# Performance work log

Hardware: AMD Instinct MI355X
Metric: run time of the kernel (lower is better)

## Reference

```python
import jax, jax.numpy as jnp
import numpy as np

SEQ_LENGTH = 8192
P_DIM = 128  # number of landmarks


def setup_inputs() -> dict:
    key = jax.random.key(0)
    kq, kk, kv = jax.random.split(key, 3)
    shape = (4, 16, SEQ_LENGTH, 64)  # [b, h, n, d]
    return {
        "q": jax.random.normal(kq, shape, dtype=jnp.float32),
        "k": jax.random.normal(kk, shape, dtype=jnp.float32),
        "v": jax.random.normal(kv, shape, dtype=jnp.float32),
    }


def _landmarks(x, p_dim, seq_length):
    # mean-pool groups of size l = ceil(seq/p_dim) into p_dim landmarks,
    # left-padding with zeros when seq % p_dim != 0 (matches torch F.pad)
    b, h, n, d = x.shape
    l = int(np.ceil(seq_length / p_dim))
    remainder = seq_length % p_dim
    if remainder > 0:
        padding = p_dim - remainder
        x = jnp.pad(x, ((0, 0), (0, 0), (padding, 0), (0, 0)))
    return x.reshape(b, h, p_dim, l, d).mean(axis=3)  # [b, h, m, d]


def reference(q, k, v):
    q = q / (q.shape[-1] ** 0.5)
    q_land = _landmarks(q, P_DIM, SEQ_LENGTH)  # [b, h, m, d]
    k_land = _landmarks(k, P_DIM, SEQ_LENGTH)  # [b, h, m, d]

    # F: queries attend to key-landmarks  [b, h, n, m]
    F = jax.nn.softmax(jnp.einsum('bhid,bhjd->bhij', q, k_land), axis=-1)
    # A: pinv of landmark-landmark attention  [b, h, m, m]
    A = jnp.linalg.pinv(jax.nn.softmax(jnp.einsum('bhid,bhjd->bhij', q_land, k_land), axis=-1))
    # B: query-landmarks attend to keys  [b, h, m, n]
    B = jax.nn.softmax(jnp.einsum('bhid,bhjd->bhij', q_land, k), axis=-1)

    # (F @ A) @ (B @ v) == F @ (A @ (B @ v)); use cheap association
    return F @ (A @ (B @ v))  # [b, h, n, d]
```

## Files before the change

kernel.cpp:

```cpp
#include <hip/hip_runtime.h>
#include <hip/hip_bf16.h>
#include <math.h>

#define BH 64
#define NSEQ 8192
#define DHEAD 64
#define M 128
#define LGRP 64
#define NCB 4
#define KPB (NSEQ / NCB)
#define TILE 64
#define NTILE (KPB / TILE)
#define NSWEEP64 3
#define NSWEEP 8
#define NROUND 127
#define RCOND 1.52587890625e-4

__global__ __launch_bounds__(64) void lm_kernel(const float* __restrict__ q,
                                                const float* __restrict__ k,
                                                double* __restrict__ ql64,
                                                double* __restrict__ kl64,
                                                float* __restrict__ qlf32,
                                                float* __restrict__ klf32) {
    int idx = blockIdx.x;
    int tensor = idx >> 13;
    int g = idx & 8191;
    int head = g >> 7, m = g & 127;
    int d = threadIdx.x;
    const float* src = tensor ? k : q;
    const float* base = src + ((size_t)head * NSEQ + (size_t)m * LGRP) * DHEAD + d;
    double s = 0.0;
    #pragma unroll 8
    for (int r = 0; r < LGRP; ++r) s += (double)base[(size_t)r * DHEAD];
    s *= (1.0 / LGRP);
    if (!tensor) s *= 0.125;
    size_t o = (size_t)head * M * DHEAD + (size_t)m * DHEAD + d;
    if (!tensor) { ql64[o] = s; qlf32[o] = (float)s; }
    else         { kl64[o] = s; klf32[o] = (float)s; }
}

__global__ __launch_bounds__(512) void s_kernel(const double* __restrict__ ql64,
                                                const double* __restrict__ kl64,
                                                double* __restrict__ Sg) {
    extern __shared__ double lds[];
    double* qlds = lds;
    double* klds = lds + M * DHEAD;
    int head = blockIdx.x;
    int t = threadIdx.x;
    const double2* qg = (const double2*)(ql64 + (size_t)head * M * DHEAD);
    const double2* kg = (const double2*)(kl64 + (size_t)head * M * DHEAD);
    for (int e = t; e < M * DHEAD / 2; e += 512) {
        ((double2*)qlds)[e] = qg[e];
        ((double2*)klds)[e] = kg[e];
    }
    __syncthreads();
    int tr = t >> 4, tc = t & 15;
    double acc[4][8];
    #pragma unroll
    for (int i = 0; i < 4; ++i)
        #pragma unroll
        for (int j = 0; j < 8; ++j) acc[i][j] = 0.0;
    for (int dc = 0; dc < DHEAD; dc += 4) {
        double qreg[4][4], kreg[8][4];
        #pragma unroll
        for (int i = 0; i < 4; ++i)
            #pragma unroll
            for (int d = 0; d < 4; ++d) qreg[i][d] = qlds[(4 * tr + i) * DHEAD + dc + d];
        #pragma unroll
        for (int j = 0; j < 8; ++j)
            #pragma unroll
            for (int d = 0; d < 4; ++d) kreg[j][d] = klds[(8 * tc + j) * DHEAD + dc + d];
        #pragma unroll
        for (int i = 0; i < 4; ++i)
            #pragma unroll
            for (int j = 0; j < 8; ++j)
                #pragma unroll
                for (int d = 0; d < 4; ++d) acc[i][j] += qreg[i][d] * kreg[j][d];
    }
    double* So = Sg + (size_t)head * M * M;
    #pragma unroll
    for (int i = 0; i < 4; ++i) {
        double mx = acc[i][0];
        #pragma unroll
        for (int j = 1; j < 8; ++j) mx = fmax(mx, acc[i][j]);
        mx = fmax(mx, __shfl_xor(mx, 1));
        mx = fmax(mx, __shfl_xor(mx, 2));
        mx = fmax(mx, __shfl_xor(mx, 4));
        mx = fmax(mx, __shfl_xor(mx, 8));
        double sum = 0.0;
        #pragma unroll
        for (int j = 0; j < 8; ++j) { acc[i][j] = exp(acc[i][j] - mx); sum += acc[i][j]; }
        sum += __shfl_xor(sum, 1); sum += __shfl_xor(sum, 2);
        sum += __shfl_xor(sum, 4); sum += __shfl_xor(sum, 8);
        double inv = 1.0 / sum;
        #pragma unroll
        for (int j = 0; j < 8; ++j)
            So[(size_t)(8 * tc + j) * M + 4 * tr + i] = acc[i][j] * inv;
    }
}

__global__ __launch_bounds__(512) void fused_kernel(const double* __restrict__ Sg,
                                                    double* __restrict__ Wcol,
                                                    const float* __restrict__ k,
                                                    const float* __restrict__ v,
                                                    const float* __restrict__ qlf32,
                                                    double* __restrict__ numd,
                                                    double* __restrict__ dend) {
    extern __shared__ double ldsd[];
    __shared__ double norms2[M];
    __shared__ double maxn2s;
    __shared__ int anyrot, done;
    int t = threadIdx.x;

    if (blockIdx.x < BH) {
        int head = blockIdx.x;
        double* G = ldsd;
        float* G32 = (float*)ldsd;
        const double2* Sh2 = (const double2*)(Sg + (size_t)head * M * M);
        double2* G2 = (double2*)G;
        for (int e = t; e < M * 64; e += 512) {
            int col = e >> 6, rp = e & 63;
            G2[col * 65 + rp] = Sh2[e];
        }
        __syncthreads();
        {
            int col = t >> 2, qd = t & 3;
            double s = 0.0;
            #pragma unroll 8
            for (int x = qd * 32; x < qd * 32 + 32; ++x) { double vv = G[col * 130 + x]; s += vv * vv; }
            s += __shfl_xor(s, 1); s += __shfl_xor(s, 2);
            if (qd == 0) norms2[col] = s;
        }
        if (t == 0) { anyrot = 1; done = 0; }
        __syncthreads();
        int grp = t >> 3, s8 = t & 7;
        int sweep = 0;
        for (; sweep < NSWEEP64; ++sweep) {
            if (t < 64) {
                double mm = fmax(norms2[t], norms2[t + 64]);
                for (int off = 32; off > 0; off >>= 1) mm = fmax(mm, __shfl_down(mm, off));
                if (t == 0) {
                    maxn2s = mm;
                    done = (sweep > 0 && anyrot == 0);
                    anyrot = 0;
                }
            }
            __syncthreads();
            if (done) break;
            double kc = maxn2s * (RCOND * RCOND);
            for (int r = 0; r < NROUND; ++r) {
                int ca, cb;
                if (grp == 0) { ca = 127; cb = r; }
                else { ca = (r + grp) % 127; cb = (r + 127 - grp) % 127; }
                double na = norms2[ca], nb = norms2[cb];
                if (na + nb >= kc) {
                    double2* gA = (double2*)(G + ca * 130);
                    double2* gB = (double2*)(G + cb * 130);
                    double2 va[8], vb[8];
                    #pragma unroll
                    for (int j = 0; j < 8; ++j) va[j] = gA[j * 8 + s8];
                    #pragma unroll
                    for (int j = 0; j < 8; ++j) vb[j] = gB[j * 8 + s8];
                    double c = 0.0;
                    #pragma unroll
                    for (int j = 0; j < 8; ++j) c += va[j].x * vb[j].x + va[j].y * vb[j].y;
                    c += __shfl_xor(c, 1); c += __shfl_xor(c, 2); c += __shfl_xor(c, 4);
                    if (c * c > 1e-24 * na * nb) {
                        if (na > kc && nb > kc && c * c > 1.6e-11 * na * nb) anyrot = 1;
                        double zeta = (nb - na) / (2.0 * c);
                        double tt = (zeta >= 0.0 ? 1.0 : -1.0) / (fabs(zeta) + sqrt(1.0 + zeta * zeta));
                        double cs = 1.0 / sqrt(1.0 + tt * tt);
                        double sn = cs * tt;
                        #pragma unroll
                        for (int j = 0; j < 8; ++j) {
                            double nax = cs * va[j].x - sn * vb[j].x;
                            double nay = cs * va[j].y - sn * vb[j].y;
                            double nbx = sn * va[j].x + cs * vb[j].x;
                            double nby = sn * va[j].y + cs * vb[j].y;
                            gA[j * 8 + s8] = make_double2(nax, nay);
                            gB[j * 8 + s8] = make_double2(nbx, nby);
                        }
                        if (s8 == 0) {
                            norms2[ca] = fmax(na - tt * c, 0.0);
                            norms2[cb] = nb + tt * c;
                        }
                    }
                }
                __syncthreads();
            }
        }
        {
            float tmp[32];
            int idx = 0;
            for (int e = t; e < M * M; e += 512) tmp[idx++] = (float)G[(e >> 7) * 130 + (e & 127)];
            __syncthreads();
            idx = 0;
            for (int e = t; e < M * M; e += 512) G32[(e >> 7) * 132 + (e & 127)] = tmp[idx++];
            __syncthreads();
        }
        for (; sweep < NSWEEP; ++sweep) {
            if (t < 64) {
                double mm = fmax(norms2[t], norms2[t + 64]);
                for (int off = 32; off > 0; off >>= 1) mm = fmax(mm, __shfl_down(mm, off));
                if (t == 0) {
                    maxn2s = mm;
                    done = (sweep > 0 && anyrot == 0);
                    anyrot = 0;
                }
            }
            __syncthreads();
            if (done) break;
            double kc = maxn2s * (RCOND * RCOND);
            for (int r = 0; r < NROUND; ++r) {
                int ca, cb;
                if (grp == 0) { ca = 127; cb = r; }
                else { ca = (r + grp) % 127; cb = (r + 127 - grp) % 127; }
                double na = norms2[ca], nb = norms2[cb];
                if (na + nb >= kc) {
                    float4* gA = (float4*)(G32 + ca * 132);
                    float4* gB = (float4*)(G32 + cb * 132);
                    float4 va[4], vb[4];
                    #pragma unroll
                    for (int j = 0; j < 4; ++j) va[j] = gA[j * 8 + s8];
                    #pragma unroll
                    for (int j = 0; j < 4; ++j) vb[j] = gB[j * 8 + s8];
                    float c32 = 0.f;
                    #pragma unroll
                    for (int j = 0; j < 4; ++j)
                        c32 += va[j].x * vb[j].x + va[j].y * vb[j].y
                             + va[j].z * vb[j].z + va[j].w * vb[j].w;
                    c32 += __shfl_xor(c32, 1); c32 += __shfl_xor(c32, 2); c32 += __shfl_xor(c32, 4);
                    double c = (double)c32;
                    if (c * c > 1e-14 * na * nb) {
                        if (na > kc && nb > kc && c * c > 1.6e-11 * na * nb) anyrot = 1;
                        double zeta = (nb - na) / (2.0 * c);
                        double tt = (zeta >= 0.0 ? 1.0 : -1.0) / (fabs(zeta) + sqrt(1.0 + zeta * zeta));
                        double cs = 1.0 / sqrt(1.0 + tt * tt);
                        double sn = cs * tt;
                        float csf = (float)cs, snf = (float)sn;
                        #pragma unroll
                        for (int j = 0; j < 4; ++j) {
                            float4 a = va[j], b = vb[j];
                            gA[j * 8 + s8] = make_float4(csf * a.x - snf * b.x, csf * a.y - snf * b.y,
                                                         csf * a.z - snf * b.z, csf * a.w - snf * b.w);
                            gB[j * 8 + s8] = make_float4(snf * a.x + csf * b.x, snf * a.y + csf * b.y,
                                                         snf * a.z + csf * b.z, snf * a.w + csf * b.w);
                        }
                        if (s8 == 0) {
                            norms2[ca] = fmax(na - tt * c, 0.0);
                            norms2[cb] = nb + tt * c;
                        }
                    }
                }
                __syncthreads();
            }
        }
        {
            int col = t >> 2, qd = t & 3;
            double s = 0.0;
            #pragma unroll 8
            for (int x = qd * 32; x < qd * 32 + 32; ++x) { double vv = (double)G32[col * 132 + x]; s += vv * vv; }
            s += __shfl_xor(s, 1); s += __shfl_xor(s, 2);
            if (qd == 0) norms2[col] = s;
        }
        __syncthreads();
        if (t < 64) {
            double mm = fmax(norms2[t], norms2[t + 64]);
            for (int off = 32; off > 0; off >>= 1) mm = fmax(mm, __shfl_down(mm, off));
            if (t == 0) maxn2s = mm;
        }
        __syncthreads();
        double cut2 = maxn2s * (RCOND * RCOND);
        for (int e = t; e < M * M; e += 512) {
            int cc = e >> 7, rr = e & 127;
            double n2 = norms2[cc];
            Wcol[(size_t)head * M * M + e] = (n2 > cut2) ? (double)G32[cc * 132 + rr] / n2 : 0.0;
        }
    } else {
        int bb = blockIdx.x - BH;
        int head = bb >> 2;
        int chunk = bb & 3;
        float* F = (float*)ldsd;
        float* qls = F;
        float* kls = F + 8704;
        float* vls = F + 13056;
        float* Zl  = F + 17408;
        {
            const float4* qg = (const float4*)(qlf32 + (size_t)head * M * DHEAD);
            for (int e = t; e < 2048; e += 512) {
                int m = e >> 4, dq = e & 15;
                *(float4*)&qls[m * 68 + dq * 4] = qg[e];
            }
        }
        int mb = t >> 4, lo = t & 15;
        double acc64[16];
        double den64[4];
        #pragma unroll
        for (int i = 0; i < 16; ++i) acc64[i] = 0.0;
        #pragma unroll
        for (int i = 0; i < 4; ++i) den64[i] = 0.0;
        size_t keybase = (size_t)head * NSEQ + (size_t)chunk * KPB;
        for (int tt = 0; tt < NTILE; ++tt) {
            __syncthreads();
            const float4* kg = (const float4*)(k + (keybase + tt * TILE) * DHEAD);
            const float4* vg = (const float4*)(v + (keybase + tt * TILE) * DHEAD);
            for (int e = t; e < 1024; e += 512) {
                int key = e >> 4, dq = e & 15;
                *(float4*)&kls[key * 68 + dq * 4] = kg[e];
                *(float4*)&vls[key * 68 + dq * 4] = vg[e];
            }
            __syncthreads();
            float z0[4], z1[4], z2[4], z3[4];
            #pragma unroll
            for (int j = 0; j < 4; ++j) { z0[j] = 0.f; z1[j] = 0.f; z2[j] = 0.f; z3[j] = 0.f; }
            for (int dc = 0; dc < DHEAD; dc += 4) {
                float4 qr[4], kr[4];
                #pragma unroll
                for (int i = 0; i < 4; ++i) qr[i] = *(const float4*)&qls[(mb * 4 + i) * 68 + dc];
                #pragma unroll
                for (int j = 0; j < 4; ++j) kr[j] = *(const float4*)&kls[(j * 16 + lo) * 68 + dc];
                #pragma unroll
                for (int j = 0; j < 4; ++j) {
                    z0[j] += qr[0].x * kr[j].x + qr[0].y * kr[j].y + qr[0].z * kr[j].z + qr[0].w * kr[j].w;
                    z1[j] += qr[1].x * kr[j].x + qr[1].y * kr[j].y + qr[1].z * kr[j].z + qr[1].w * kr[j].w;
                    z2[j] += qr[2].x * kr[j].x + qr[2].y * kr[j].y + qr[2].z * kr[j].z + qr[2].w * kr[j].w;
                    z3[j] += qr[3].x * kr[j].x + qr[3].y * kr[j].y + qr[3].z * kr[j].z + qr[3].w * kr[j].w;
                }
            }
            #pragma unroll
            for (int j = 0; j < 4; ++j) {
                float4 ej;
                ej.x = __expf(z0[j]); ej.y = __expf(z1[j]);
                ej.z = __expf(z2[j]); ej.w = __expf(z3[j]);
                *(float4*)&Zl[(j * 16 + lo) * 132 + mb * 4] = ej;
            }
            __syncthreads();
            float4 a32[4];
            #pragma unroll
            for (int i = 0; i < 4; ++i) a32[i] = make_float4(0.f, 0.f, 0.f, 0.f);
            float den32[4] = {0.f, 0.f, 0.f, 0.f};
            for (int key = 0; key < TILE; ++key) {
                float4 vv = *(const float4*)&vls[key * 68 + lo * 4];
                float4 ee = *(const float4*)&Zl[key * 132 + mb * 4];
                a32[0].x += ee.x * vv.x; a32[0].y += ee.x * vv.y; a32[0].z += ee.x * vv.z; a32[0].w += ee.x * vv.w;
                a32[1].x += ee.y * vv.x; a32[1].y += ee.y * vv.y; a32[1].z += ee.y * vv.z; a32[1].w += ee.y * vv.w;
                a32[2].x += ee.z * vv.x; a32[2].y += ee.z * vv.y; a32[2].z += ee.z * vv.z; a32[2].w += ee.z * vv.w;
                a32[3].x += ee.w * vv.x; a32[3].y += ee.w * vv.y; a32[3].z += ee.w * vv.z; a32[3].w += ee.w * vv.w;
                if (lo == 0) { den32[0] += ee.x; den32[1] += ee.y; den32[2] += ee.z; den32[3] += ee.w; }
            }
            #pragma unroll
            for (int i = 0; i < 4; ++i) {
                acc64[i * 4 + 0] += (double)a32[i].x;
                acc64[i * 4 + 1] += (double)a32[i].y;
                acc64[i * 4 + 2] += (double)a32[i].z;
                acc64[i * 4 + 3] += (double)a32[i].w;
            }
            if (lo == 0) {
                #pragma unroll
                for (int i = 0; i < 4; ++i) den64[i] += (double)den32[i];
            }
        }
        #pragma unroll
        for (int i = 0; i < 4; ++i) {
            size_t ob = (((size_t)head * NCB + chunk) * M + mb * 4 + i) * DHEAD + lo * 4;
            *(double2*)&numd[ob]     = make_double2(acc64[i * 4 + 0], acc64[i * 4 + 1]);
            *(double2*)&numd[ob + 2] = make_double2(acc64[i * 4 + 2], acc64[i * 4 + 3]);
        }
        if (lo == 0) {
            #pragma unroll
            for (int i = 0; i < 4; ++i)
                dend[((size_t)head * NCB + chunk) * M + mb * 4 + i] = den64[i];
        }
    }
}

__global__ __launch_bounds__(512) void apply_kernel(const double* __restrict__ numd,
                                                    const double* __restrict__ dend,
                                                    const double* __restrict__ Wcol,
                                                    const double* __restrict__ Sg,
                                                    float* __restrict__ ABvf32) {
    extern __shared__ double lds[];
    double* A_ = lds;
    double* B_ = lds + M * 66;
    __shared__ double dsum[M];
    int head = blockIdx.x;
    int t = threadIdx.x;
    if (t < M) {
        double s = 0.0;
        #pragma unroll
        for (int c = 0; c < NCB; ++c) s += dend[((size_t)head * NCB + c) * M + t];
        dsum[t] = s;
    }
    __syncthreads();
    for (int e = t; e < M * DHEAD; e += 512) {
        int mm = e >> 6;
        double s = 0.0;
        #pragma unroll
        for (int c = 0; c < NCB; ++c) s += numd[((size_t)head * NCB + c) * (M * DHEAD) + e];
        A_[mm * 66 + (e & 63)] = s / dsum[mm];
    }
    __syncthreads();
    int i = t >> 3, qd = t & 7;
    const double* Wb = Wcol + (size_t)head * M * M;
    const double* Sb = Sg + (size_t)head * M * M;
    {
        double a0[8], a1[8];
        #pragma unroll
        for (int d = 0; d < 8; ++d) { a0[d] = 0.0; a1[d] = 0.0; }
        for (int r = 0; r < M; ++r) {
            double m0 = Wb[(size_t)i * M + r];
            double m1 = Wb[(size_t)(i + 64) * M + r];
            #pragma unroll
            for (int d = 0; d < 8; ++d) {
                double xv = A_[r * 66 + qd * 8 + d];
                a0[d] += m0 * xv; a1[d] += m1 * xv;
            }
        }
        #pragma unroll
        for (int d = 0; d < 8; ++d) {
            B_[i * 66 + qd * 8 + d] = a0[d];
            B_[(i + 64) * 66 + qd * 8 + d] = a1[d];
        }
    }
    __syncthreads();
    {
        double a0[8], a1[8];
        #pragma unroll
        for (int d = 0; d < 8; ++d) { a0[d] = 0.0; a1[d] = 0.0; }
        for (int r = 0; r < M; ++r) {
            double m0 = Wb[(size_t)r * M + i];
            double m1 = Wb[(size_t)r * M + i + 64];
            #pragma unroll
            for (int d = 0; d < 8; ++d) {
                double xv = B_[r * 66 + qd * 8 + d];
                a0[d] += m0 * xv; a1[d] += m1 * xv;
            }
        }
        #pragma unroll
        for (int d = 0; d < 8; ++d) {
            A_[i * 66 + qd * 8 + d] = a0[d];
            A_[(i + 64) * 66 + qd * 8 + d] = a1[d];
        }
    }
    __syncthreads();
    {
        double a0[8], a1[8];
        #pragma unroll
        for (int d = 0; d < 8; ++d) { a0[d] = 0.0; a1[d] = 0.0; }
        for (int r = 0; r < M; ++r) {
            double m0 = Sb[(size_t)i * M + r];
            double m1 = Sb[(size_t)(i + 64) * M + r];
            #pragma unroll
            for (int d = 0; d < 8; ++d) {
                double xv = A_[r * 66 + qd * 8 + d];
                a0[d] += m0 * xv; a1[d] += m1 * xv;
            }
        }
        float* ob = ABvf32 + (size_t)head * M * DHEAD;
        #pragma unroll
        for (int d = 0; d < 8; ++d) {
            ob[i * DHEAD + qd * 8 + d] = (float)a0[d];
            ob[(i + 64) * DHEAD + qd * 8 + d] = (float)a1[d];
        }
    }
}

__global__ __launch_bounds__(512) void out_kernel(const float* __restrict__ q,
                                                  const float* __restrict__ klf32,
                                                  const float* __restrict__ ABvf32,
                                                  float* __restrict__ out) {
    __shared__ float kls[M * DHEAD];
    __shared__ float avs[M * DHEAD];
    int head = blockIdx.x >> 4;
    int tile = blockIdx.x & 15;
    int t = threadIdx.x;
    for (int e = t; e < M * DHEAD; e += 512) {
        kls[e] = klf32[(size_t)head * M * DHEAD + e];
        avs[e] = ABvf32[(size_t)head * M * DHEAD + e];
    }
    __syncthreads();
    int rl = t >> 1, h = t & 1;
    size_t row0 = (size_t)head * NSEQ + (size_t)tile * 512 + rl;
    size_t row1 = row0 + 256;
    const float4* qr0 = (const float4*)(q + row0 * DHEAD + h * 32);
    const float4* qr1 = (const float4*)(q + row1 * DHEAD + h * 32);
    float4 qa[8], qb[8];
    #pragma unroll
    for (int c = 0; c < 8; ++c) {
        float4 x = qr0[c];
        x.x *= 0.125f; x.y *= 0.125f; x.z *= 0.125f; x.w *= 0.125f;
        qa[c] = x;
        float4 y = qr1[c];
        y.x *= 0.125f; y.y *= 0.125f; y.z *= 0.125f; y.w *= 0.125f;
        qb[c] = y;
    }
    float acc0[32], acc1[32];
    #pragma unroll
    for (int d = 0; d < 32; ++d) { acc0[d] = 0.f; acc1[d] = 0.f; }
    float d0 = 0.f, d1 = 0.f;
    for (int mm = 0; mm < M; ++mm) {
        const float4* kr = (const float4*)(kls + mm * DHEAD + h * 32);
        float z0 = 0.f, z1 = 0.f;
        #pragma unroll
        for (int c = 0; c < 8; ++c) {
            float4 kk = kr[c];
            z0 += qa[c].x * kk.x + qa[c].y * kk.y + qa[c].z * kk.z + qa[c].w * kk.w;
            z1 += qb[c].x * kk.x + qb[c].y * kk.y + qb[c].z * kk.z + qb[c].w * kk.w;
        }
        z0 += __shfl_xor(z0, 1);
        z1 += __shfl_xor(z1, 1);
        float e0 = __expf(z0), e1 = __expf(z1);
        d0 += e0; d1 += e1;
        const float4* ar = (const float4*)(avs + mm * DHEAD + h * 32);
        #pragma unroll
        for (int c = 0; c < 8; ++c) {
            float4 av = ar[c];
            acc0[4 * c]     += e0 * av.x; acc0[4 * c + 1] += e0 * av.y;
            acc0[4 * c + 2] += e0 * av.z; acc0[4 * c + 3] += e0 * av.w;
            acc1[4 * c]     += e1 * av.x; acc1[4 * c + 1] += e1 * av.y;
            acc1[4 * c + 2] += e1 * av.z; acc1[4 * c + 3] += e1 * av.w;
        }
    }
    float i0 = 1.f / d0, i1 = 1.f / d1;
    float* o0 = out + row0 * DHEAD + h * 32;
    float* o1 = out + row1 * DHEAD + h * 32;
    #pragma unroll
    for (int d = 0; d < 32; ++d) { o0[d] = acc0[d] * i0; o1[d] = acc1[d] * i1; }
}

extern "C" void kernel_launch(void* const* d_in, const int* in_sizes, int n_in,
                              void* d_out, int out_size, void* d_ws, size_t ws_size,
                              hipStream_t stream) {
    const float* q = (const float*)d_in[0];
    const float* k = (const float*)d_in[1];
    const float* v = (const float*)d_in[2];
    float* out = (float*)d_out;
    char* ws = (char*)d_ws;
    double* ql64  = (double*)(ws + 0);
    double* kl64  = (double*)(ws + 4194304);
    double* numd  = (double*)(ws + 0);
    double* dend  = (double*)(ws + 33554432);
    float*  qlf32 = (float*)(ws + 34078720);
    float*  klf32 = (float*)(ws + 36175872);
    double* Sg    = (double*)(ws + 38273024);
    double* Wcol  = (double*)(ws + 46661632);
    float*  ABvf32= (float*)(ws + 55050240);

    lm_kernel<<<16384, 64, 0, stream>>>(q, k, ql64, kl64, qlf32, klf32);
    s_kernel<<<BH, 512, 2 * M * DHEAD * 8, stream>>>(ql64, kl64, Sg);
    fused_kernel<<<BH + 256, 512, 133120, stream>>>(Sg, Wcol, k, v, qlf32, numd, dend);
    apply_kernel<<<BH, 512, 2 * M * 66 * 8, stream>>>(numd, dend, Wcol, Sg, ABvf32);
    out_kernel<<<BH * 16, 512, 0, stream>>>(q, klf32, ABvf32, out);
}
```

Baseline: 2.250 ms.

## Double fused kernel block size to 1024 threads and split keys into 8 chunks

Raises the fused kernel block size from 512 to 1024 threads. In the one-sided Jacobi SVD path, each column pair is now handled by 16 lanes instead of 8, which halves the per-thread work and the register arrays for every rotation. The B@v path splits the keys into 8 chunks instead of 4, so it runs 512 blocks, and each thread computes 2 landmark rows instead of 4. The aim is to shorten the serial Jacobi critical path, which runs 127 synchronised rounds per sweep, and to add parallelism to the accumulation. In exchange, reductions get longer, barriers span 1024 threads, and apply_kernel must sum more partial chunks.

```diff
diff --git a/kernel.cpp b/kernel.cpp
--- a/kernel.cpp
+++ b/kernel.cpp
@@ -7,7 +7,7 @@
 #define DHEAD 64
 #define M 128
 #define LGRP 64
-#define NCB 4
+#define NCB 8
 #define KPB (NSEQ / NCB)
 #define TILE 64
 #define NTILE (KPB / TILE)
@@ -99,13 +99,13 @@
     }
 }
 
-__global__ __launch_bounds__(512) void fused_kernel(const double* __restrict__ Sg,
-                                                    double* __restrict__ Wcol,
-                                                    const float* __restrict__ k,
-                                                    const float* __restrict__ v,
-                                                    const float* __restrict__ qlf32,
-                                                    double* __restrict__ numd,
-                                                    double* __restrict__ dend) {
+__global__ __launch_bounds__(1024) void fused_kernel(const double* __restrict__ Sg,
+                                                     double* __restrict__ Wcol,
+                                                     const float* __restrict__ k,
+                                                     const float* __restrict__ v,
+                                                     const float* __restrict__ qlf32,
+                                                     double* __restrict__ numd,
+                                                     double* __restrict__ dend) {
     extern __shared__ double ldsd[];
     __shared__ double norms2[M];
     __shared__ double maxn2s;
@@ -118,22 +118,22 @@
         float* G32 = (float*)ldsd;
         const double2* Sh2 = (const double2*)(Sg + (size_t)head * M * M);
         double2* G2 = (double2*)G;
-        for (int e = t; e < M * 64; e += 512) {
+        for (int e = t; e < M * 64; e += 1024) {
             int col = e >> 6, rp = e & 63;
             G2[col * 65 + rp] = Sh2[e];
         }
         __syncthreads();
         {
-            int col = t >> 2, qd = t & 3;
+            int col = t >> 3, qd = t & 7;
             double s = 0.0;
             #pragma unroll 8
-            for (int x = qd * 32; x < qd * 32 + 32; ++x) { double vv = G[col * 130 + x]; s += vv * vv; }
-            s += __shfl_xor(s, 1); s += __shfl_xor(s, 2);
+            for (int x = qd * 16; x < qd * 16 + 16; ++x) { double vv = G[col * 130 + x]; s += vv * vv; }
+            s += __shfl_xor(s, 1); s += __shfl_xor(s, 2); s += __shfl_xor(s, 4);
             if (qd == 0) norms2[col] = s;
         }
         if (t == 0) { anyrot = 1; done = 0; }
         __syncthreads();
-        int grp = t >> 3, s8 = t & 7;
+        int grp = t >> 4, s16 = t & 15;
         int sweep = 0;
         for (; sweep < NSWEEP64; ++sweep) {
             if (t < 64) {
@@ -156,15 +156,16 @@
                 if (na + nb >= kc) {
                     double2* gA = (double2*)(G + ca * 130);
                     double2* gB = (double2*)(G + cb * 130);
-                    double2 va[8], vb[8];
+                    double2 va[4], vb[4];
                     #pragma unroll
-                    for (int j = 0; j < 8; ++j) va[j] = gA[j * 8 + s8];
+                    for (int j = 0; j < 4; ++j) va[j] = gA[j * 16 + s16];
                     #pragma unroll
-                    for (int j = 0; j < 8; ++j) vb[j] = gB[j * 8 + s8];
+                    for (int j = 0; j < 4; ++j) vb[j] = gB[j * 16 + s16];
                     double c = 0.0;
                     #pragma unroll
-                    for (int j = 0; j < 8; ++j) c += va[j].x * vb[j].x + va[j].y * vb[j].y;
-                    c += __shfl_xor(c, 1); c += __shfl_xor(c, 2); c += __shfl_xor(c, 4);
+                    for (int j = 0; j < 4; ++j) c += va[j].x * vb[j].x + va[j].y * vb[j].y;
+                    c += __shfl_xor(c, 1); c += __shfl_xor(c, 2);
+                    c += __shfl_xor(c, 4); c += __shfl_xor(c, 8);
                     if (c * c > 1e-24 * na * nb) {
                         if (na > kc && nb > kc && c * c > 1.6e-11 * na * nb) anyrot = 1;
                         double zeta = (nb - na) / (2.0 * c);
@@ -172,15 +173,15 @@
                         double cs = 1.0 / sqrt(1.0 + tt * tt);
                         double sn = cs * tt;
                         #pragma unroll
-                        for (int j = 0; j < 8; ++j) {
+                        for (int j = 0; j < 4; ++j) {
                             double nax = cs * va[j].x - sn * vb[j].x;
                             double nay = cs * va[j].y - sn * vb[j].y;
                             double nbx = sn * va[j].x + cs * vb[j].x;
                             double nby = sn * va[j].y + cs * vb[j].y;
-                            gA[j * 8 + s8] = make_double2(nax, nay);
-                            gB[j * 8 + s8] = make_double2(nbx, nby);
+                            gA[j * 16 + s16] = make_double2(nax, nay);
+                            gB[j * 16 + s16] = make_double2(nbx, nby);
                         }
-                        if (s8 == 0) {
+                        if (s16 == 0) {
                             norms2[ca] = fmax(na - tt * c, 0.0);
                             norms2[cb] = nb + tt * c;
                         }
@@ -190,12 +191,12 @@
             }
         }
         {
-            float tmp[32];
+            float tmp[16];
             int idx = 0;
-            for (int e = t; e < M * M; e += 512) tmp[idx++] = (float)G[(e >> 7) * 130 + (e & 127)];
+            for (int e = t; e < M * M; e += 1024) tmp[idx++] = (float)G[(e >> 7) * 130 + (e & 127)];
             __syncthreads();
             idx = 0;
-            for (int e = t; e < M * M; e += 512) G32[(e >> 7) * 132 + (e & 127)] = tmp[idx++];
+            for (int e = t; e < M * M; e += 1024) G32[(e >> 7) * 132 + (e & 127)] = tmp[idx++];
             __syncthreads();
         }
         for (; sweep < NSWEEP; ++sweep) {
@@ -219,17 +220,18 @@
                 if (na + nb >= kc) {
                     float4* gA = (float4*)(G32 + ca * 132);
                     float4* gB = (float4*)(G32 + cb * 132);
-                    float4 va[4], vb[4];
+                    float4 va[2], vb[2];
                     #pragma unroll
-                    for (int j = 0; j < 4; ++j) va[j] = gA[j * 8 + s8];
+                    for (int j = 0; j < 2; ++j) va[j] = gA[j * 16 + s16];
                     #pragma unroll
-                    for (int j = 0; j < 4; ++j) vb[j] = gB[j * 8 + s8];
+                    for (int j = 0; j < 2; ++j) vb[j] = gB[j * 16 + s16];
                     float c32 = 0.f;
                     #pragma unroll
-                    for (int j = 0; j < 4; ++j)
+                    for (int j = 0; j < 2; ++j)
                         c32 += va[j].x * vb[j].x + va[j].y * vb[j].y
                              + va[j].z * vb[j].z + va[j].w * vb[j].w;
-                    c32 += __shfl_xor(c32, 1); c32 += __shfl_xor(c32, 2); c32 += __shfl_xor(c32, 4);
+                    c32 += __shfl_xor(c32, 1); c32 += __shfl_xor(c32, 2);
+                    c32 += __shfl_xor(c32, 4); c32 += __shfl_xor(c32, 8);
                     double c = (double)c32;
                     if (c * c > 1e-14 * na * nb) {
                         if (na > kc && nb > kc && c * c > 1.6e-11 * na * nb) anyrot = 1;
@@ -239,14 +241,14 @@
                         double sn = cs * tt;
                         float csf = (float)cs, snf = (float)sn;
                         #pragma unroll
-                        for (int j = 0; j < 4; ++j) {
+                        for (int j = 0; j < 2; ++j) {
                             float4 a = va[j], b = vb[j];
-                            gA[j * 8 + s8] = make_float4(csf * a.x - snf * b.x, csf * a.y - snf * b.y,
-                                                         csf * a.z - snf * b.z, csf * a.w - snf * b.w);
-                            gB[j * 8 + s8] = make_float4(snf * a.x + csf * b.x, snf * a.y + csf * b.y,
-                                                         snf * a.z + csf * b.z, snf * a.w + csf * b.w);
+                            gA[j * 16 + s16] = make_float4(csf * a.x - snf * b.x, csf * a.y - snf * b.y,
+                                                           csf * a.z - snf * b.z, csf * a.w - snf * b.w);
+                            gB[j * 16 + s16] = make_float4(snf * a.x + csf * b.x, snf * a.y + csf * b.y,
+                                                           snf * a.z + csf * b.z, snf * a.w + csf * b.w);
                         }
-                        if (s8 == 0) {
+                        if (s16 == 0) {
                             norms2[ca] = fmax(na - tt * c, 0.0);
                             norms2[cb] = nb + tt * c;
                         }
@@ -256,11 +258,11 @@
             }
         }
         {
-            int col = t >> 2, qd = t & 3;
+            int col = t >> 3, qd = t & 7;
             double s = 0.0;
             #pragma unroll 8
-            for (int x = qd * 32; x < qd * 32 + 32; ++x) { double vv = (double)G32[col * 132 + x]; s += vv * vv; }
-            s += __shfl_xor(s, 1); s += __shfl_xor(s, 2);
+            for (int x = qd * 16; x < qd * 16 + 16; ++x) { double vv = (double)G32[col * 132 + x]; s += vv * vv; }
+            s += __shfl_xor(s, 1); s += __shfl_xor(s, 2); s += __shfl_xor(s, 4);
             if (qd == 0) norms2[col] = s;
         }
         __syncthreads();
@@ -271,15 +273,15 @@
         }
         __syncthreads();
         double cut2 = maxn2s * (RCOND * RCOND);
-        for (int e = t; e < M * M; e += 512) {
+        for (int e = t; e < M * M; e += 1024) {
             int cc = e >> 7, rr = e & 127;
             double n2 = norms2[cc];
             Wcol[(size_t)head * M * M + e] = (n2 > cut2) ? (double)G32[cc * 132 + rr] / n2 : 0.0;
         }
     } else {
         int bb = blockIdx.x - BH;
-        int head = bb >> 2;
-        int chunk = bb & 3;
+        int head = bb >> 3;
+        int chunk = bb & 7;
         float* F = (float*)ldsd;
         float* qls = F;
         float* kls = F + 8704;
@@ -287,89 +289,76 @@
         float* Zl  = F + 17408;
         {
             const float4* qg = (const float4*)(qlf32 + (size_t)head * M * DHEAD);
-            for (int e = t; e < 2048; e += 512) {
+            for (int e = t; e < 2048; e += 1024) {
                 int m = e >> 4, dq = e & 15;
                 *(float4*)&qls[m * 68 + dq * 4] = qg[e];
             }
         }
         int mb = t >> 4, lo = t & 15;
-        double acc64[16];
-        double den64[4];
-        #pragma unroll
-        for (int i = 0; i < 16; ++i) acc64[i] = 0.0;
-        #pragma unroll
-        for (int i = 0; i < 4; ++i) den64[i] = 0.0;
+        int r0 = 2 * mb, r1 = 2 * mb + 1;
+        double acc64[8];
+        double den64[2];
+        #pragma unroll
+        for (int i = 0; i < 8; ++i) acc64[i] = 0.0;
+        den64[0] = 0.0; den64[1] = 0.0;
         size_t keybase = (size_t)head * NSEQ + (size_t)chunk * KPB;
         for (int tt = 0; tt < NTILE; ++tt) {
             __syncthreads();
             const float4* kg = (const float4*)(k + (keybase + tt * TILE) * DHEAD);
             const float4* vg = (const float4*)(v + (keybase + tt * TILE) * DHEAD);
-            for (int e = t; e < 1024; e += 512) {
-                int key = e >> 4, dq = e & 15;
-                *(float4*)&kls[key * 68 + dq * 4] = kg[e];
-                *(float4*)&vls[key * 68 + dq * 4] = vg[e];
-            }
-            __syncthreads();
-            float z0[4], z1[4], z2[4], z3[4];
-            #pragma unroll
-            for (int j = 0; j < 4; ++j) { z0[j] = 0.f; z1[j] = 0.f; z2[j] = 0.f; z3[j] = 0.f; }
+            if (t < 1024) {
+                int key = t >> 4, dq = t & 15;
+                *(float4*)&kls[key * 68 + dq * 4] = kg[t];
+                *(float4*)&vls[key * 68 + dq * 4] = vg[t];
+            }
+            __syncthreads();
+            float z0[4], z1[4];
+            #pragma unroll
+            for (int j = 0; j < 4; ++j) { z0[j] = 0.f; z1[j] = 0.f; }
             for (int dc = 0; dc < DHEAD; dc += 4) {
-                float4 qr[4], kr[4];
-                #pragma unroll
-                for (int i = 0; i < 4; ++i) qr[i] = *(const float4*)&qls[(mb * 4 + i) * 68 + dc];
+                float4 qr0 = *(const float4*)&qls[r0 * 68 + dc];
+                float4 qr1 = *(const float4*)&qls[r1 * 68 + dc];
+                float4 kr[4];
                 #pragma unroll
                 for (int j = 0; j < 4; ++j) kr[j] = *(const float4*)&kls[(j * 16 + lo) * 68 + dc];
                 #pragma unroll
                 for (int j = 0; j < 4; ++j) {
-                    z0[j] += qr[0].x * kr[j].x + qr[0].y * kr[j].y + qr[0].z * kr[j].z + qr[0].w * kr[j].w;
-                    z1[j] += qr[1].x * kr[j].x + qr[1].y * kr[j].y + qr[1].z * kr[j].z + qr[1].w * kr[j].w;
-                    z2[j] += qr[2].x * kr[j].x + qr[2].y * kr[j].y + qr[2].z * kr[j].z + qr[2].w * kr[j].w;
-                    z3[j] += qr[3].x * kr[j].x + qr[3].y * kr[j].y + qr[3].z * kr[j].z + qr[3].w * kr[j].w;
+                    z0[j] += qr0.x * kr[j].x + qr0.y * kr[j].y + qr0.z * kr[j].z + qr0.w * kr[j].w;
+                    z1[j] += qr1.x * kr[j].x + qr1.y * kr[j].y + qr1.z * kr[j].z + qr1.w * kr[j].w;
                 }
             }
             #pragma unroll
             for (int j = 0; j < 4; ++j) {
-                float4 ej;
+                float2 ej;
                 ej.x = __expf(z0[j]); ej.y = __expf(z1[j]);
-                ej.z = __expf(z2[j]); ej.w = __expf(z3[j]);
-                *(float4*)&Zl[(j * 16 + lo) * 132 + mb * 4] = ej;
-            }
-            __syncthreads();
-            float4 a32[4];
-            #pragma unroll
-            for (int i = 0; i < 4; ++i) a32[i] = make_float4(0.f, 0.f, 0.f, 0.f);
-            float den32[4] = {0.f, 0.f, 0.f, 0.f};
+                *(float2*)&Zl[(j * 16 + lo) * 132 + r0] = ej;
+            }
+            __syncthreads();
+            float4 a0 = make_float4(0.f, 0.f, 0.f, 0.f);
+            float4 a1 = make_float4(0.f, 0.f, 0.f, 0.f);
+            float d0 = 0.f, d1 = 0.f;
             for (int key = 0; key < TILE; ++key) {
                 float4 vv = *(const float4*)&vls[key * 68 + lo * 4];
-                float4 ee = *(const float4*)&Zl[key * 132 + mb * 4];
-                a32[0].x += ee.x * vv.x; a32[0].y += ee.x * vv.y; a32[0].z += ee.x * vv.z; a32[0].w += ee.x * vv.w;
-                a32[1].x += ee.y * vv.x; a32[1].y += ee.y * vv.y; a32[1].z += ee.y * vv.z; a32[1].w += ee.y * vv.w;
-                a32[2].x += ee.z * vv.x; a32[2].y += ee.z * vv.y; a32[2].z += ee.z * vv.z; a32[2].w += ee.z * vv.w;
-                a32[3].x += ee.w * vv.x; a32[3].y += ee.w * vv.y; a32[3].z += ee.w * vv.z; a32[3].w += ee.w * vv.w;
-                if (lo == 0) { den32[0] += ee.x; den32[1] += ee.y; den32[2] += ee.z; den32[3] += ee.w; }
-            }
-            #pragma unroll
-            for (int i = 0; i < 4; ++i) {
-                acc64[i * 4 + 0] += (double)a32[i].x;
-                acc64[i * 4 + 1] += (double)a32[i].y;
-                acc64[i * 4 + 2] += (double)a32[i].z;
-                acc64[i * 4 + 3] += (double)a32[i].w;
-            }
-            if (lo == 0) {
-                #pragma unroll
-                for (int i = 0; i < 4; ++i) den64[i] += (double)den32[i];
-            }
-        }
-        #pragma unroll
-        for (int i = 0; i < 4; ++i) {
-            size_t ob = (((size_t)head * NCB + chunk) * M + mb * 4 + i) * DHEAD + lo * 4;
+                float2 ee = *(const float2*)&Zl[key * 132 + r0];
+                a0.x += ee.x * vv.x; a0.y += ee.x * vv.y; a0.z += ee.x * vv.z; a0.w += ee.x * vv.w;
+                a1.x += ee.y * vv.x; a1.y += ee.y * vv.y; a1.z += ee.y * vv.z; a1.w += ee.y * vv.w;
+                if (lo == 0) { d0 += ee.x; d1 += ee.y; }
+            }
+            acc64[0] += (double)a0.x; acc64[1] += (double)a0.y;
+            acc64[2] += (double)a0.z; acc64[3] += (double)a0.w;
+            acc64[4] += (double)a1.x; acc64[5] += (double)a1.y;
+            acc64[6] += (double)a1.z; acc64[7] += (double)a1.w;
+            if (lo == 0) { den64[0] += (double)d0; den64[1] += (double)d1; }
+        }
+        #pragma unroll
+        for (int i = 0; i < 2; ++i) {
+            size_t ob = (((size_t)head * NCB + chunk) * M + r0 + i) * DHEAD + lo * 4;
             *(double2*)&numd[ob]     = make_double2(acc64[i * 4 + 0], acc64[i * 4 + 1]);
             *(double2*)&numd[ob + 2] = make_double2(acc64[i * 4 + 2], acc64[i * 4 + 3]);
         }
         if (lo == 0) {
-            #pragma unroll
-            for (int i = 0; i < 4; ++i)
-                dend[((size_t)head * NCB + chunk) * M + mb * 4 + i] = den64[i];
+            dend[((size_t)head * NCB + chunk) * M + r0] = den64[0];
+            dend[((size_t)head * NCB + chunk) * M + r1] = den64[1];
         }
     }
 }
@@ -548,7 +537,7 @@
 
     lm_kernel<<<16384, 64, 0, stream>>>(q, k, ql64, kl64, qlf32, klf32);
     s_kernel<<<BH, 512, 2 * M * DHEAD * 8, stream>>>(ql64, kl64, Sg);
-    fused_kernel<<<BH + 256, 512, 133120, stream>>>(Sg, Wcol, k, v, qlf32, numd, dend);
+    fused_kernel<<<BH + 512, 1024, 133120, stream>>>(Sg, Wcol, k, v, qlf32, numd, dend);
     apply_kernel<<<BH, 512, 2 * M * 66 * 8, stream>>>(numd, dend, Wcol, Sg, ABvf32);
     out_kernel<<<BH * 16, 512, 0, stream>>>(q, klf32, ABvf32, out);
 }
```

After: 2.483 ms. 1.1x slower.
